# Kernel tuning notes

Measured on AMD Instinct MI355X. Metric: run time of the kernel, lower is better.

## Reference

```python
import jax, jax.numpy as jnp
import numpy as np

EPS = 1e-12

def _l2norm(v):
    # torch.nn.functional.normalize(p=2) with eps clamp
    return v / jnp.maximum(jnp.linalg.norm(v), EPS)

def _spectral_weight(W, U):
    # W: (out, in) flattened 1x1 conv weight; U: (1, out) power-iteration buffer.
    # One power iteration, all under stop_gradient (torch.no_grad in original).
    V = _l2norm(U @ W)            # (1, in)
    Unew = _l2norm(V @ W.T)       # (1, out)
    sigma = (Unew @ W @ V.T)[0, 0]
    return W / jax.lax.stop_gradient(sigma)

def _conv1x1(x, W, b):
    # x: (b,c,h,w), W: (o,c), b: (o,)
    return jnp.einsum('oc,bchw->bohw', W, x) + b[None, :, None, None]

def setup_inputs() -> dict:
    key = jax.random.key(0)
    ks = jax.random.split(key, 11)
    B, C, H, W = 4, 256, 64, 64
    Ck = C // 8
    return {
        'x':   jax.random.normal(ks[0], (B, C, H, W), jnp.float32),
        'f_w': jax.random.normal(ks[1], (Ck, C), jnp.float32) * 0.05,
        'f_b': jax.random.normal(ks[2], (Ck,), jnp.float32) * 0.05,
        'f_u': jax.random.uniform(ks[3], (1, Ck), jnp.float32),
        'g_w': jax.random.normal(ks[4], (Ck, C), jnp.float32) * 0.05,
        'g_b': jax.random.normal(ks[5], (Ck,), jnp.float32) * 0.05,
        'g_u': jax.random.uniform(ks[6], (1, Ck), jnp.float32),
        'h_w': jax.random.normal(ks[7], (C, C), jnp.float32) * 0.05,
        'h_b': jax.random.normal(ks[8], (C,), jnp.float32) * 0.05,
        'h_u': jax.random.uniform(ks[9], (1, C), jnp.float32),
        'gamma': jax.random.normal(ks[10], (1, 1), jnp.float32),
    }

def reference(x, f_w, f_b, f_u, g_w, g_b, g_u, h_w, h_b, h_u, gamma):
    b, c, h, w = x.shape
    hw = h * w
    key_ = _conv1x1(x, _spectral_weight(f_w, f_u), f_b).reshape(b, -1, hw).transpose(0, 2, 1)  # (b,hw,ck)
    query = _conv1x1(x, _spectral_weight(g_w, g_u), g_b).reshape(b, -1, hw)                    # (b,ck,hw)
    attn = jax.nn.softmax(jnp.einsum('bnd,bdm->bnm', key_, query), axis=-1)                    # (b,hw,hw)
    value = _conv1x1(x, _spectral_weight(h_w, h_u), h_b).reshape(b, -1, hw)                    # (b,c,hw)
    out = jnp.einsum('bnm,bcm->bnc', attn, value)                                              # (b,hw,c)
    # Faithful to original: raw view of (b,hw,c) contiguous buffer into (b,c,h,w)
    out = out.reshape(b, c, h, w)
    return gamma[0, 0] * out + x
```

## Files before the change

### kernel.cpp

```cpp
#include <hip/hip_runtime.h>


constexpr int kC   = 256;
constexpr int kHW  = 4096;
constexpr int kB   = 4;
constexpr int kCHW = kC * kHW;

typedef short bf16x8 __attribute__((ext_vector_type(8)));
typedef float f32x4  __attribute__((ext_vector_type(4)));
typedef unsigned short u16;

#if __has_builtin(__builtin_amdgcn_exp2f)
#define EXP2(x) __builtin_amdgcn_exp2f(x)
#else
#define EXP2(x) exp2f(x)
#endif

__device__ __forceinline__ u16 f2bf(float f) {
    union { float f; unsigned u; } v; v.f = f;
    unsigned u = v.u;
    return (u16)((u + 0x7fffu + ((u >> 16) & 1u)) >> 16);
}
__device__ __forceinline__ float bf2f(u16 h) {
    union { unsigned u; float f; } v; v.u = ((unsigned)h) << 16;
    return v.f;
}

__global__ __launch_bounds__(1024) void k_prep(
    const float* __restrict__ fw, const float* __restrict__ fu,
    const float* __restrict__ gw, const float* __restrict__ gu,
    const float* __restrict__ hww, const float* __restrict__ hu,
    float* __restrict__ sig, u16* __restrict__ wh, u16* __restrict__ wl)
{
    if (blockIdx.x >= 3) {
        const int tid = (blockIdx.x - 3) * 1024 + threadIdx.x;
        const int g  = tid >> 8;
        const int ci = tid & 255;
        const float f = (g < 32) ? fw[g * 256 + ci]
                      : (g < 64) ? gw[(g - 32) * 256 + ci]
                                 : hww[(g - 64) * 256 + ci];
        const int idx = ((g >> 4) * 8 + (ci >> 5)) * 512 + (g & 15) * 32 + (ci & 31);
        const u16 h = f2bf(f);
        wh[idx] = h;
        wl[idx] = f2bf(f - bf2f(h));
        return;
    }

    const int which = blockIdx.x;
    const float* W = which == 0 ? fw : (which == 1 ? gw : hww);
    const float* U = which == 0 ? fu : (which == 1 ? gu : hu);
    const int O = (which == 2) ? 256 : 32;
    const int t = threadIdx.x;

    __shared__ float par[4][256];
    __shared__ float red[256];
    __shared__ __align__(16) float Vv[256];

    {
        const int i = t & 255, och = t >> 8;
        float p = 0.f;
        if (O == 256) {
            const float* Wc = W + (size_t)(och * 64) * 256 + i;
            const float* Uc = U + och * 64;
#pragma unroll 8
            for (int oo = 0; oo < 64; ++oo)
                p += Uc[oo] * Wc[(size_t)oo * 256];
        } else if (och == 0) {
            const float* Wc = W + i;
#pragma unroll 8
            for (int oo = 0; oo < 32; ++oo)
                p += U[oo] * Wc[(size_t)oo * 256];
        }
        par[och][i] = p;
    }
    __syncthreads();
    float t1 = 0.f;
    if (t < 256) {
        t1 = par[0][t] + par[1][t] + par[2][t] + par[3][t];
        red[t] = t1 * t1;
    }
    __syncthreads();
    for (int s = 128; s > 0; s >>= 1) { if (t < s) red[t] += red[t + s]; __syncthreads(); }
    if (t < 256) Vv[t] = t1 / fmaxf(sqrtf(red[0]), 1e-12f);
    __syncthreads();

    {
        const int o = t & 255, ich = t >> 8;
        float q = 0.f;
        if (o < O) {
            const float4* Wr = (const float4*)(W + (size_t)o * 256 + ich * 64);
            const float4* Vr = (const float4*)(&Vv[ich * 64]);
#pragma unroll
            for (int j = 0; j < 16; ++j) {
                const float4 w = Wr[j]; const float4 v = Vr[j];
                q += w.x * v.x + w.y * v.y + w.z * v.z + w.w * v.w;
            }
        }
        par[ich][o] = q;
    }
    __syncthreads();
    if (t < 256) {
        const float t2 = par[0][t] + par[1][t] + par[2][t] + par[3][t];
        red[t] = t2 * t2;
    }
    __syncthreads();
    for (int s = 128; s > 0; s >>= 1) { if (t < s) red[t] += red[t + s]; __syncthreads(); }
    if (t == 0) {
        const float s2 = red[0];
        sig[which] = fmaxf(sqrtf(s2), 1e-12f) / s2;
    }
}

__global__ __launch_bounds__(512) void k_proj(
    const float* __restrict__ x,
    const u16* __restrict__ wh, const u16* __restrict__ wl,
    const float* __restrict__ fb, const float* __restrict__ gb,
    const float* __restrict__ hb, const float* __restrict__ sig,
    u16* __restrict__ Kc, u16* __restrict__ Qc, u16* __restrict__ Vb)
{
    __shared__ __align__(16) float xs[256][64];
    __shared__ float bLDS[320];

    const int t = threadIdx.x;
    const int wave = t >> 6, lane = t & 63;
    const int quad = lane >> 4, l15 = lane & 15;
    const int b = blockIdx.y;
    const int n0 = blockIdx.x * 64;
    const int nch = wave & 3, cohalf = wave >> 2;

    constexpr float kLog2e = 1.44269504f;

    {
        const int r4i = lane >> 4, c16 = lane & 15;
        const float* xg = x + (size_t)b * kCHW + (size_t)r4i * kHW + n0 + c16 * 4;
#pragma unroll
        for (int j = 0; j < 8; ++j) {
            const int cibase = (wave * 8 + j) * 4;
            __builtin_amdgcn_global_load_lds(
                (const __attribute__((address_space(1))) void*)(xg + (size_t)cibase * kHW),
                (__attribute__((address_space(3))) void*)&xs[cibase][0], 16, 0, 0);
        }
    }
    if (t < 320) bLDS[t] = (t < 32) ? fb[t]
                         : (t < 64) ? gb[t - 32] * kLog2e
                         : hb[t - 64];
    __syncthreads();

    const int n = nch * 16 + l15;
    bf16x8 bh[8], bl[8];
#pragma unroll
    for (int s = 0; s < 8; ++s) {
        union { u16 a[8]; bf16x8 v; } H, L;
#pragma unroll
        for (int j = 0; j < 8; ++j) {
            const float v = xs[s * 32 + quad * 8 + j][n];
            const u16 h = f2bf(v);
            H.a[j] = h; L.a[j] = f2bf(v - bf2f(h));
        }
        bh[s] = H.v; bl[s] = L.v;
    }

    const u16* whp = wh + l15 * 32 + quad * 8;
    const u16* wlp = wl + l15 * 32 + quad * 8;

    f32x4 acc[10] = {};
#pragma unroll
    for (int c = 0; c < 10; ++c) {
        const size_t base = (size_t)(cohalf * 10 + c) * 4096;
#pragma unroll
        for (int s = 0; s < 8; ++s) {
            const bf16x8 ah = *(const bf16x8*)(whp + base + s * 512);
            const bf16x8 al = *(const bf16x8*)(wlp + base + s * 512);
            acc[c] = __builtin_amdgcn_mfma_f32_16x16x32_bf16(ah, bh[s], acc[c], 0, 0, 0);
            acc[c] = __builtin_amdgcn_mfma_f32_16x16x32_bf16(ah, bl[s], acc[c], 0, 0, 0);
            acc[c] = __builtin_amdgcn_mfma_f32_16x16x32_bf16(al, bh[s], acc[c], 0, 0, 0);
        }
    }

    const float s0 = sig[0], s1 = sig[1] * kLog2e, s2 = sig[2];
#pragma unroll
    for (int c = 0; c < 10; ++c) {
        const int cog0 = (cohalf * 10 + c) * 16;
        const float inv = (cog0 < 32) ? s0 : (cog0 < 64) ? s1 : s2;
        if (cog0 < 64) {
            u16 hi[4], lo[4];
#pragma unroll
            for (int r = 0; r < 4; ++r) {
                const float v = acc[c][r] * inv + bLDS[cog0 + quad * 4 + r];
                hi[r] = f2bf(v);
                lo[r] = f2bf(v - bf2f(hi[r]));
            }
            u16* H = (cog0 < 32) ? Kc : Qc;
            const int dbase = (cog0 & 31) + quad * 4;
            const size_t off = (size_t)(b * kHW + n0 + n) * 64;
            const unsigned h01 = (unsigned)hi[0] | ((unsigned)hi[1] << 16);
            const unsigned h23 = (unsigned)hi[2] | ((unsigned)hi[3] << 16);
            const unsigned l01 = (unsigned)lo[0] | ((unsigned)lo[1] << 16);
            const unsigned l23 = (unsigned)lo[2] | ((unsigned)lo[3] << 16);
            *(uint2*)(H + off + dbase)      = make_uint2(h01, h23);
            *(uint2*)(H + off + 32 + dbase) = make_uint2(l01, l23);
        } else {
#pragma unroll
            for (int r = 0; r < 4; ++r) {
                const int co = cog0 + quad * 4 + r;
                const float v = acc[c][r] * inv + bLDS[co];
                Vb[((size_t)b * kC + (co - 64)) * kHW + n0 + n] = f2bf(v);
            }
        }
    }
}

__global__ __launch_bounds__(512, 4) void k_attn(
    const u16* __restrict__ Kc, const u16* __restrict__ Qc,
    const u16* __restrict__ Vb,
    u16* __restrict__ Op, float* __restrict__ Sl)
{
    __shared__ __align__(16) u16 Qt[2][4096];
    __shared__ __align__(16) u16 Pt[3][4096];
    __shared__ float lsum[8][16];

    const int t = threadIdx.x;
    const int wave = t >> 6, lane = t & 63;
    const int quad = lane >> 4, l15 = lane & 15;
    const int sg = wave >> 1, half = wave & 1;

    const int id = blockIdx.x;
    const int xcd = id & 7;
    const int b = xcd >> 1;
    const int nb0 = ((xcd & 1) * 32 + ((id >> 3) & 31)) * 64;
    const int mh = id >> 8;
    const int mt0 = mh * 32, mt1 = mt0 + 32;

    const u16* Kb  = Kc + (size_t)b * kHW * 64;
    const u16* Qb  = Qc + (size_t)b * kHW * 64;
    const u16* Vbb = Vb + (size_t)b * kC * kHW;

    const size_t krow = (size_t)(nb0 + sg * 16 + l15) * 64 + (size_t)quad * 8;
    const bf16x8 kh = *(const bf16x8*)(Kb + krow);
    const bf16x8 kl = *(const bf16x8*)(Kb + krow + 32);

    const u16* vrow[2];
#pragma unroll
    for (int ct = 0; ct < 2; ++ct)
        vrow[ct] = Vbb + (size_t)(wave * 32 + ct * 16 + l15) * kHW + quad * 8;

    const int qs_row = lane >> 3, qs_ch = lane & 7;
    const int rloc = wave * 8 + qs_row;
    const int qswz = (qs_ch ^ (rloc & 7)) << 3;

    f32x4 O[8] = {};
    float lrow = 0.f;
    bf16x8 vc[4], vn[4];

#define QK_TILE(buf, sdst)                                                        \
    {                                                                             \
        __builtin_amdgcn_s_setprio(1);                                            \
        _Pragma("unroll")                                                         \
        for (int mi2 = 0; mi2 < 2; ++mi2) {                                       \
            const int mi = half * 2 + mi2;                                        \
            const int rbase = (mi * 16 + l15) * 64;                               \
            const bf16x8 qhv = *(const bf16x8*)&Qt[buf][rbase + ((quad       ^ (l15 & 7)) << 3)]; \
            const bf16x8 qlv = *(const bf16x8*)&Qt[buf][rbase + (((quad + 4) ^ (l15 & 7)) << 3)]; \
            f32x4 a = { 0.f, 0.f, 0.f, 0.f };                                     \
            a = __builtin_amdgcn_mfma_f32_16x16x32_bf16(qhv, kl, a, 0, 0, 0);     \
            a = __builtin_amdgcn_mfma_f32_16x16x32_bf16(qlv, kh, a, 0, 0, 0);     \
            a = __builtin_amdgcn_mfma_f32_16x16x32_bf16(qhv, kh, a, 0, 0, 0);     \
            sdst[mi2] = a;                                                        \
        }                                                                         \
        __builtin_amdgcn_s_setprio(0);                                            \
    }

#define PACK_TILE(pi, ssrc)                                                       \
    {                                                                             \
        const int prow = sg * 16 + l15;                                           \
        _Pragma("unroll")                                                         \
        for (int mi2 = 0; mi2 < 2; ++mi2) {                                       \
            const float p0 = EXP2(ssrc[mi2][0]);                                  \
            const float p1 = EXP2(ssrc[mi2][1]);                                  \
            const float p2 = EXP2(ssrc[mi2][2]);                                  \
            const float p3 = EXP2(ssrc[mi2][3]);                                  \
            lrow += (p0 + p1) + (p2 + p3);                                        \
            const unsigned d0 = __builtin_amdgcn_perm(                            \
                __float_as_uint(p1), __float_as_uint(p0), 0x07060302u);           \
            const unsigned d1 = __builtin_amdgcn_perm(                            \
                __float_as_uint(p3), __float_as_uint(p2), 0x07060302u);           \
            const int mi = half * 2 + mi2;                                        \
            const int chunk = 2 * mi + (quad >> 1);                               \
            const int off = prow * 64 + ((chunk ^ (l15 & 7)) << 3) + (quad & 1) * 4; \
            *(uint2*)(Pt[pi] + off) = make_uint2(d0, d1);                         \
        }                                                                         \
    }

#define PV_TILE(pi, vsrc)                                                         \
    {                                                                             \
        __builtin_amdgcn_s_setprio(1);                                            \
        _Pragma("unroll")                                                         \
        for (int ks = 0; ks < 2; ++ks) {                                          \
            _Pragma("unroll")                                                     \
            for (int rg = 0; rg < 4; ++rg) {                                      \
                const bf16x8 pa = *(const bf16x8*)&Pt[pi][(rg * 16 + l15) * 64    \
                                     + (((ks * 4 + quad) ^ (l15 & 7)) << 3)];     \
                _Pragma("unroll")                                                 \
                for (int ct = 0; ct < 2; ++ct)                                    \
                    O[rg * 2 + ct] = __builtin_amdgcn_mfma_f32_16x16x32_bf16(     \
                        pa, vsrc[ct * 2 + ks], O[rg * 2 + ct], 0, 0, 0);          \
            }                                                                     \
        }                                                                         \
        __builtin_amdgcn_s_setprio(0);                                            \
    }

    __builtin_amdgcn_global_load_lds(
        (const __attribute__((address_space(1))) void*)
            (Qb + (size_t)(mt0 * 64 + rloc) * 64 + qswz),
        (__attribute__((address_space(3))) void*)&Qt[0][wave * 512], 16, 0, 0);
    __syncthreads();

    {
        __builtin_amdgcn_global_load_lds(
            (const __attribute__((address_space(1))) void*)
                (Qb + (size_t)((mt0 + 1) * 64 + rloc) * 64 + qswz),
            (__attribute__((address_space(3))) void*)&Qt[1][wave * 512], 16, 0, 0);
#pragma unroll
        for (int ct = 0; ct < 2; ++ct)
#pragma unroll
            for (int ks = 0; ks < 2; ++ks)
                vc[ct * 2 + ks] = *(const bf16x8*)(vrow[ct] + mt0 * 64 + ks * 32);
        f32x4 s[2];
        QK_TILE(0, s);
        PACK_TILE(mt0 % 3, s);
        __syncthreads();
    }

    for (int mt = mt0 + 1; mt < mt1; ++mt) {
        const int cur = mt & 1;
        const int pi = mt % 3;
        const int pprev = (mt + 2) % 3;
        const int m0 = mt * 64;

        if (mt < mt1 - 1) {
            __builtin_amdgcn_global_load_lds(
                (const __attribute__((address_space(1))) void*)
                    (Qb + (size_t)(m0 + 64 + rloc) * 64 + qswz),
                (__attribute__((address_space(3))) void*)&Qt[cur ^ 1][wave * 512], 16, 0, 0);
        }
#pragma unroll
        for (int ct = 0; ct < 2; ++ct)
#pragma unroll
            for (int ks = 0; ks < 2; ++ks)
                vn[ct * 2 + ks] = *(const bf16x8*)(vrow[ct] + m0 + ks * 32);

        f32x4 s[2];
        QK_TILE(cur, s);
        PACK_TILE(pi, s);
        PV_TILE(pprev, vc);

        __syncthreads();

#pragma unroll
        for (int i = 0; i < 4; ++i) vc[i] = vn[i];
    }

    PV_TILE((mt1 - 1) % 3, vc);

#undef QK_TILE
#undef PACK_TILE
#undef PV_TILE

    lrow += __shfl_xor(lrow, 16);
    lrow += __shfl_xor(lrow, 32);
    if (lane < 16) lsum[wave][l15] = lrow;
    __syncthreads();
    if (half == 0 && lane < 16)
        Sl[(size_t)(mh * 4 + b) * kHW + nb0 + sg * 16 + l15]
            = lsum[wave][l15] + lsum[wave ^ 1][l15];

    u16* Opb = Op + (size_t)(mh * 4 + b) * kHW * 256;
#pragma unroll
    for (int rg = 0; rg < 4; ++rg) {
#pragma unroll
        for (int ct = 0; ct < 2; ++ct) {
#pragma unroll
            for (int r = 0; r < 4; ++r) {
                const int nn = nb0 + rg * 16 + quad * 4 + r;
                const int c = wave * 32 + ct * 16 + l15;
                Opb[(size_t)nn * 256 + c] = f2bf(O[rg * 2 + ct][r]);
            }
        }
    }
}

__global__ __launch_bounds__(256) void k_merge(
    const float* __restrict__ x, const float* __restrict__ gamma,
    const u16* __restrict__ Op, const float* __restrict__ Sl,
    float* __restrict__ out)
{
    const int tid = blockIdx.x * 256 + threadIdx.x;
    const int cg = tid & 31;
    const int n  = (tid >> 5) & 4095;
    const int b  = tid >> 17;
    const int c0 = cg * 8;

    const float la = Sl[(size_t)b * kHW + n];
    const float lb = Sl[(size_t)(4 + b) * kHW + n];
    const float invL = 1.f / (la + lb);
    const float g = gamma[0];

    const size_t base = ((size_t)b * kHW + n) * 256 + c0;
    const uint4 A = *(const uint4*)(Op + base);
    const uint4 B = *(const uint4*)(Op + base + (size_t)4 * kHW * 256);
    const float4 x0 = *(const float4*)(x + base);
    const float4 x1 = *(const float4*)(x + base + 4);

    float o[8];
    const unsigned aw[4] = { A.x, A.y, A.z, A.w };
    const unsigned bw[4] = { B.x, B.y, B.z, B.w };
#pragma unroll
    for (int j = 0; j < 8; ++j) {
        const float va = bf2f((u16)(aw[j >> 1] >> ((j & 1) * 16)));
        const float vb = bf2f((u16)(bw[j >> 1] >> ((j & 1) * 16)));
        o[j] = (va + vb) * invL;
    }
    float4 r0, r1;
    r0.x = g * o[0] + x0.x; r0.y = g * o[1] + x0.y;
    r0.z = g * o[2] + x0.z; r0.w = g * o[3] + x0.w;
    r1.x = g * o[4] + x1.x; r1.y = g * o[5] + x1.y;
    r1.z = g * o[6] + x1.z; r1.w = g * o[7] + x1.w;
    *(float4*)(out + base)     = r0;
    *(float4*)(out + base + 4) = r1;
}

extern "C" void kernel_launch(void* const* d_in, const int* in_sizes, int n_in,
                              void* d_out, int out_size, void* d_ws, size_t ws_size,
                              hipStream_t stream)
{
    const float* x     = (const float*)d_in[0];
    const float* fw    = (const float*)d_in[1];
    const float* fb    = (const float*)d_in[2];
    const float* fu    = (const float*)d_in[3];
    const float* gw    = (const float*)d_in[4];
    const float* gb    = (const float*)d_in[5];
    const float* gu    = (const float*)d_in[6];
    const float* hww   = (const float*)d_in[7];
    const float* hb    = (const float*)d_in[8];
    const float* hu    = (const float*)d_in[9];
    const float* gamma = (const float*)d_in[10];
    float* out = (float*)d_out;

    char* ws = (char*)d_ws;
    float* sig = (float*)ws;
    u16* wh = (u16*)(ws + 1024);
    u16* wl = wh + 320 * 256;
    u16* Kc = (u16*)(ws + (1u << 20));
    u16* Qc = (u16*)(ws + (3u << 20));
    u16* Vb = (u16*)(ws + (5u << 20));
    u16* Op = (u16*)(ws + (16u << 20));
    float* Sl = (float*)(ws + (32u << 20));

    k_prep<<<dim3(83), dim3(1024), 0, stream>>>(fw, fu, gw, gu, hww, hu, sig, wh, wl);
    k_proj<<<dim3(64, 4), dim3(512), 0, stream>>>(x, wh, wl, fb, gb, hb, sig,
                                                  Kc, Qc, Vb);
    k_attn<<<dim3(512), dim3(512), 0, stream>>>(Kc, Qc, Vb, Op, Sl);
    k_merge<<<dim3(2048), dim3(256), 0, stream>>>(x, gamma, Op, Sl, out);
}
```

Baseline: 218.0 us.

## Process two key tiles per iteration to halve attention-loop barriers

Restructures the attention main loop so each iteration handles two 64-wide m-tiles. Q is staged two tiles at a time, P is double-buffered, and there is one barrier per pair. This replaces the previous software pipeline, in which PV of tile t-1 overlapped with QK of tile t under a triple-buffered P. The aim is to cut the number of __syncthreads and loop overhead. The costs are losing the QK/PV overlap across the barrier, more LDS use (Qt and Pt grow to 4 tiles each), and more registers for the two V fragments, which may reduce occupancy.

```diff
diff --git a/kernel.cpp b/kernel.cpp
--- a/kernel.cpp
+++ b/kernel.cpp
@@ -215,8 +215,8 @@
     const u16* __restrict__ Vb,
     u16* __restrict__ Op, float* __restrict__ Sl)
 {
-    __shared__ __align__(16) u16 Qt[2][4096];
-    __shared__ __align__(16) u16 Pt[3][4096];
+    __shared__ __align__(16) u16 Qt[2][2][4096];
+    __shared__ __align__(16) u16 Pt[2][2][4096];
     __shared__ float lsum[8][16];
 
     const int t = threadIdx.x;
@@ -229,7 +229,7 @@
     const int b = xcd >> 1;
     const int nb0 = ((xcd & 1) * 32 + ((id >> 3) & 31)) * 64;
     const int mh = id >> 8;
-    const int mt0 = mh * 32, mt1 = mt0 + 32;
+    const int mt0 = mh * 32;
 
     const u16* Kb  = Kc + (size_t)b * kHW * 64;
     const u16* Qb  = Qc + (size_t)b * kHW * 64;
@@ -250,17 +250,23 @@
 
     f32x4 O[8] = {};
     float lrow = 0.f;
-    bf16x8 vc[4], vn[4];
-
-#define QK_TILE(buf, sdst)                                                        \
+    bf16x8 vc0[4], vc1[4];
+
+#define STAGE_Q(buf, tt, mt)                                                      \
+    __builtin_amdgcn_global_load_lds(                                             \
+        (const __attribute__((address_space(1))) void*)                           \
+            (Qb + (size_t)((mt) * 64 + rloc) * 64 + qswz),                        \
+        (__attribute__((address_space(3))) void*)&Qt[buf][tt][wave * 512], 16, 0, 0)
+
+#define QK_TILE(buf, tt, sdst)                                                    \
     {                                                                             \
         __builtin_amdgcn_s_setprio(1);                                            \
         _Pragma("unroll")                                                         \
         for (int mi2 = 0; mi2 < 2; ++mi2) {                                       \
             const int mi = half * 2 + mi2;                                        \
             const int rbase = (mi * 16 + l15) * 64;                               \
-            const bf16x8 qhv = *(const bf16x8*)&Qt[buf][rbase + ((quad       ^ (l15 & 7)) << 3)]; \
-            const bf16x8 qlv = *(const bf16x8*)&Qt[buf][rbase + (((quad + 4) ^ (l15 & 7)) << 3)]; \
+            const bf16x8 qhv = *(const bf16x8*)&Qt[buf][tt][rbase + ((quad       ^ (l15 & 7)) << 3)]; \
+            const bf16x8 qlv = *(const bf16x8*)&Qt[buf][tt][rbase + (((quad + 4) ^ (l15 & 7)) << 3)]; \
             f32x4 a = { 0.f, 0.f, 0.f, 0.f };                                     \
             a = __builtin_amdgcn_mfma_f32_16x16x32_bf16(qhv, kl, a, 0, 0, 0);     \
             a = __builtin_amdgcn_mfma_f32_16x16x32_bf16(qlv, kh, a, 0, 0, 0);     \
@@ -270,7 +276,7 @@
         __builtin_amdgcn_s_setprio(0);                                            \
     }
 
-#define PACK_TILE(pi, ssrc)                                                       \
+#define PACK_TILE(buf, tt, ssrc)                                                  \
     {                                                                             \
         const int prow = sg * 16 + l15;                                           \
         _Pragma("unroll")                                                         \
@@ -287,18 +293,18 @@
             const int mi = half * 2 + mi2;                                        \
             const int chunk = 2 * mi + (quad >> 1);                               \
             const int off = prow * 64 + ((chunk ^ (l15 & 7)) << 3) + (quad & 1) * 4; \
-            *(uint2*)(Pt[pi] + off) = make_uint2(d0, d1);                         \
+            *(uint2*)(Pt[buf][tt] + off) = make_uint2(d0, d1);                    \
         }                                                                         \
     }
 
-#define PV_TILE(pi, vsrc)                                                         \
+#define PV_TILE(buf, tt, vsrc)                                                    \
     {                                                                             \
         __builtin_amdgcn_s_setprio(1);                                            \
         _Pragma("unroll")                                                         \
         for (int ks = 0; ks < 2; ++ks) {                                          \
             _Pragma("unroll")                                                     \
             for (int rg = 0; rg < 4; ++rg) {                                      \
-                const bf16x8 pa = *(const bf16x8*)&Pt[pi][(rg * 16 + l15) * 64    \
+                const bf16x8 pa = *(const bf16x8*)&Pt[buf][tt][(rg * 16 + l15) * 64 \
                                      + (((ks * 4 + quad) ^ (l15 & 7)) << 3)];     \
                 _Pragma("unroll")                                                 \
                 for (int ct = 0; ct < 2; ++ct)                                    \
@@ -309,59 +315,42 @@
         __builtin_amdgcn_s_setprio(0);                                            \
     }
 
-    __builtin_amdgcn_global_load_lds(
-        (const __attribute__((address_space(1))) void*)
-            (Qb + (size_t)(mt0 * 64 + rloc) * 64 + qswz),
-        (__attribute__((address_space(3))) void*)&Qt[0][wave * 512], 16, 0, 0);
-    __syncthreads();
-
-    {
-        __builtin_amdgcn_global_load_lds(
-            (const __attribute__((address_space(1))) void*)
-                (Qb + (size_t)((mt0 + 1) * 64 + rloc) * 64 + qswz),
-            (__attribute__((address_space(3))) void*)&Qt[1][wave * 512], 16, 0, 0);
-#pragma unroll
-        for (int ct = 0; ct < 2; ++ct)
-#pragma unroll
-            for (int ks = 0; ks < 2; ++ks)
-                vc[ct * 2 + ks] = *(const bf16x8*)(vrow[ct] + mt0 * 64 + ks * 32);
-        f32x4 s[2];
-        QK_TILE(0, s);
-        PACK_TILE(mt0 % 3, s);
+    STAGE_Q(0, 0, mt0);
+    STAGE_Q(0, 1, mt0 + 1);
+    __syncthreads();
+
+    for (int j = 0; j < 16; ++j) {
+        const int buf = j & 1;
+        const int mt = mt0 + 2 * j;
+
+        if (j < 15) {
+            STAGE_Q(buf ^ 1, 0, mt + 2);
+            STAGE_Q(buf ^ 1, 1, mt + 3);
+        }
+        {
+            const int m0a = mt * 64, m0b = m0a + 64;
+#pragma unroll
+            for (int ct = 0; ct < 2; ++ct)
+#pragma unroll
+                for (int ks = 0; ks < 2; ++ks) {
+                    vc0[ct * 2 + ks] = *(const bf16x8*)(vrow[ct] + m0a + ks * 32);
+                    vc1[ct * 2 + ks] = *(const bf16x8*)(vrow[ct] + m0b + ks * 32);
+                }
+        }
+
+        f32x4 s0[2], s1[2];
+        QK_TILE(buf, 0, s0);
+        QK_TILE(buf, 1, s1);
+        PACK_TILE(buf, 0, s0);
+        PACK_TILE(buf, 1, s1);
+
         __syncthreads();
-    }
-
-    for (int mt = mt0 + 1; mt < mt1; ++mt) {
-        const int cur = mt & 1;
-        const int pi = mt % 3;
-        const int pprev = (mt + 2) % 3;
-        const int m0 = mt * 64;
-
-        if (mt < mt1 - 1) {
-            __builtin_amdgcn_global_load_lds(
-                (const __attribute__((address_space(1))) void*)
-                    (Qb + (size_t)(m0 + 64 + rloc) * 64 + qswz),
-                (__attribute__((address_space(3))) void*)&Qt[cur ^ 1][wave * 512], 16, 0, 0);
-        }
-#pragma unroll
-        for (int ct = 0; ct < 2; ++ct)
-#pragma unroll
-            for (int ks = 0; ks < 2; ++ks)
-                vn[ct * 2 + ks] = *(const bf16x8*)(vrow[ct] + m0 + ks * 32);
-
-        f32x4 s[2];
-        QK_TILE(cur, s);
-        PACK_TILE(pi, s);
-        PV_TILE(pprev, vc);
-
-        __syncthreads();
-
-#pragma unroll
-        for (int i = 0; i < 4; ++i) vc[i] = vn[i];
-    }
-
-    PV_TILE((mt1 - 1) % 3, vc);
-
+
+        PV_TILE(buf, 0, vc0);
+        PV_TILE(buf, 1, vc1);
+    }
+
+#undef STAGE_Q
 #undef QK_TILE
 #undef PACK_TILE
 #undef PV_TILE
```

Result: slower. 227.3 us (+4.3%).
